# Kernel tuning notes

Hardware: AMD Instinct MI355X
Metric: run time of the kernel (lower is better)

## Reference

```python
import jax, jax.numpy as jnp
import numpy as np

B, S, D, H = 1, 4096, 768, 12
HD = D // H
FF = 4 * D
EPS = 1e-5


def _layer_norm(x, w, b):
    mu = jnp.mean(x, axis=-1, keepdims=True)
    var = jnp.mean((x - mu) ** 2, axis=-1, keepdims=True)
    return (x - mu) * jax.lax.rsqrt(var + EPS) * w + b


def setup_inputs() -> dict:
    key = jax.random.key(0)
    ks = jax.random.split(key, 16)
    s = 0.02
    inp = {
        "hidden_states": jax.random.normal(ks[0], (B, S, D), jnp.float32),
        "attention_mask": jnp.ones((B, S), jnp.int32),
        "ln1_w": jnp.ones((D,), jnp.float32),
        "ln1_b": jnp.zeros((D,), jnp.float32),
        "wq": jax.random.normal(ks[1], (D, D), jnp.float32) * s,
        "bq": jnp.zeros((D,), jnp.float32),
        "wk": jax.random.normal(ks[2], (D, D), jnp.float32) * s,
        "bk": jnp.zeros((D,), jnp.float32),
        "wv": jax.random.normal(ks[3], (D, D), jnp.float32) * s,
        "bv": jnp.zeros((D,), jnp.float32),
        "wo": jax.random.normal(ks[4], (D, D), jnp.float32) * s,
        "bo": jnp.zeros((D,), jnp.float32),
        "ln2_w": jnp.ones((D,), jnp.float32),
        "ln2_b": jnp.zeros((D,), jnp.float32),
        "w_up": jax.random.normal(ks[5], (D, FF), jnp.float32) * s,
        "b_up": jnp.zeros((FF,), jnp.float32),
        "w_down": jax.random.normal(ks[6], (FF, D), jnp.float32) * s,
        "b_down": jnp.zeros((D,), jnp.float32),
    }
    return inp


def reference(hidden_states, attention_mask, ln1_w, ln1_b, wq, bq, wk, bk, wv, bv,
              wo, bo, ln2_w, ln2_b, w_up, b_up, w_down, b_down):
    b, s, _ = hidden_states.shape
    residual = hidden_states
    x = _layer_norm(hidden_states, ln1_w, ln1_b)
    # projections; weights stored [in, out]
    q = (x @ wq + bq).reshape(b, s, H, HD).transpose(0, 2, 1, 3)  # (b,h,s,hd)
    k = (x @ wk + bk).reshape(b, s, H, HD).transpose(0, 2, 1, 3)
    v = (x @ wv + bv).reshape(b, s, H, HD).transpose(0, 2, 1, 3)
    scores = jnp.einsum("bhqd,bhkd->bhqk", q, k) / np.float32(np.sqrt(HD))
    causal = jnp.triu(jnp.ones((s, s), bool), k=1)  # True above diagonal -> mask
    neg_inf = jnp.float32(-jnp.inf)
    scores = jnp.where(causal[None, None, :, :], neg_inf, scores)
    pad = (attention_mask[:, None, None, :] == 0)
    scores = jnp.where(pad, neg_inf, scores)
    weights = jax.nn.softmax(scores, axis=-1)
    attn = jnp.einsum("bhqk,bhkd->bhqd", weights, v)
    attn = attn.transpose(0, 2, 1, 3).reshape(b, s, D)
    hidden = residual + (attn @ wo + bo)
    # FFN
    residual = hidden
    y = _layer_norm(hidden, ln2_w, ln2_b)
    y = jax.nn.gelu(y @ w_up + b_up, approximate=False)
    y = y @ w_down + b_down
    return residual + y
```

## Files before the change

### kernel.cpp

```cpp
#include <hip/hip_runtime.h>
#include <cstdint>
#include <cstddef>


#define S_  4096
#define D_  768
#define H_  12
#define HD_ 64
#define FF_ 3072
#define SD_ (4096 * 768)

typedef short  short8  __attribute__((ext_vector_type(8)));
typedef float  floatx4 __attribute__((ext_vector_type(4)));

__device__ __forceinline__ float bf2f(unsigned short h) {
  union { unsigned int u; float f; } v; v.u = ((unsigned int)h) << 16; return v.f;
}
__device__ __forceinline__ unsigned short f2bf(float f) {
  union { unsigned int u; float f; } v; v.f = f;
  unsigned int u = v.u;
  return (unsigned short)((u + 0x7FFFu + ((u >> 16) & 1u)) >> 16);
}
__device__ __forceinline__ unsigned short f2bf_fast(float f) {
  union { unsigned int u; float f; } v; v.f = f;
  return (unsigned short)((v.u + 0x8000u) >> 16);
}
__device__ __forceinline__ void gload_lds16(const unsigned short* g, unsigned short* l) {
  __builtin_amdgcn_global_load_lds(
      (const __attribute__((address_space(1))) unsigned int*)g,
      (__attribute__((address_space(3))) unsigned int*)l, 16, 0, 0);
}

__global__ void k_cvt_f32(const void* __restrict__ src, float* __restrict__ dst,
                          int n, const int* __restrict__ flagp) {
  const int flag = *flagp;
  for (int i = blockIdx.x * blockDim.x + threadIdx.x; i < n; i += gridDim.x * blockDim.x)
    dst[i] = flag ? ((const float*)src)[i] : bf2f(((const unsigned short*)src)[i]);
}

__global__ __launch_bounds__(256) void k_cvt_t6(
    const void* s0, const void* s1, const void* s2, const void* s3,
    const void* s4, const void* s5,
    unsigned short* d0, unsigned short* d1, unsigned short* d2,
    unsigned short* d3, unsigned short* d4, unsigned short* d5,
    const int* __restrict__ flagp) {
  __shared__ unsigned short T[64 * 65];
  const int flag = *flagp;
  const int b = blockIdx.x;
  const void* src; unsigned short* dst; int K, N, ti;
  if (b < 576) {
    const int seg = b / 144; ti = b - seg * 144; K = 768; N = 768;
    const void* ss[4] = {s0, s1, s2, s3};
    unsigned short* dd[4] = {d0, d1, d2, d3};
    src = ss[seg]; dst = dd[seg];
  } else if (b < 1152) { ti = b - 576;  K = 768;  N = 3072; src = s4; dst = d4; }
  else                 { ti = b - 1152; K = 3072; N = 768;  src = s5; dst = d5; }
  const int nx = N >> 6;
  const int n0 = (ti % nx) * 64, k0 = (ti / nx) * 64;
  const int t = threadIdx.x;
  const int cl = t & 63, rg = t >> 6;
#pragma unroll
  for (int i = 0; i < 16; ++i) {
    const int kl = rg * 16 + i;
    const size_t si = (size_t)(k0 + kl) * N + n0 + cl;
    T[kl * 65 + cl] = flag ? f2bf(((const float*)src)[si]) : ((const unsigned short*)src)[si];
  }
  __syncthreads();
#pragma unroll
  for (int i = 0; i < 16; ++i) {
    const int nl = rg * 16 + i;
    dst[(size_t)(n0 + nl) * K + k0 + cl] = T[cl * 65 + nl];
  }
}

__global__ void k_cvt_params(const void* p0, const void* p1, const void* p2, const void* p3,
                             const void* p4, const void* p5, const void* p6, const void* p7,
                             const void* p8, const void* p9,
                             float* __restrict__ dst, int* __restrict__ flagp) {
  const int flag = (((const unsigned int*)p0)[0] == 0x3F800000u) ? 1 : 0;
  int i = blockIdx.x * 256 + threadIdx.x;
  if (i == 0) *flagp = flag;
  if (i >= 9984) return;
  const void* src; int j;
  if (i < 6912) {
    int seg = i / 768; j = i - seg * 768;
    const void* tbl[9] = {p0, p1, p2, p3, p4, p5, p6, p7, p8};
    src = tbl[seg];
  } else { src = p9; j = i - 6912; }
  dst[i] = flag ? ((const float*)src)[j] : bf2f(((const unsigned short*)src)[j]);
}

__global__ __launch_bounds__(256) void k_ln(const float* __restrict__ x,
                                            const float* __restrict__ w,
                                            const float* __restrict__ b,
                                            unsigned short* __restrict__ out,
                                            const float* __restrict__ bias2,
                                            float* __restrict__ acc) {
  const int row = blockIdx.x, t = threadIdx.x;
  const float* xr = x + (size_t)row * D_;
  float v0 = xr[t], v1 = xr[t + 256], v2 = xr[t + 512];
  float s = v0 + v1 + v2;
  float ss = v0 * v0 + v1 * v1 + v2 * v2;
  for (int off = 32; off > 0; off >>= 1) {
    s  += __shfl_down(s, off);
    ss += __shfl_down(ss, off);
  }
  __shared__ float sb[4], ssb[4];
  const int wid = t >> 6, lane = t & 63;
  if (lane == 0) { sb[wid] = s; ssb[wid] = ss; }
  __syncthreads();
  s  = sb[0] + sb[1] + sb[2] + sb[3];
  ss = ssb[0] + ssb[1] + ssb[2] + ssb[3];
  const float mu   = s * (1.0f / D_);
  const float var  = ss * (1.0f / D_) - mu * mu;
  const float rstd = rsqrtf(var + 1e-5f);
  unsigned short* orow = out + (size_t)row * D_;
  orow[t]       = f2bf((v0 - mu) * rstd * w[t]       + b[t]);
  orow[t + 256] = f2bf((v1 - mu) * rstd * w[t + 256] + b[t + 256]);
  orow[t + 512] = f2bf((v2 - mu) * rstd * w[t + 512] + b[t + 512]);
  if (acc) {
    float* arow = acc + (size_t)row * D_;
    arow[t]       = v0 + bias2[t];
    arow[t + 256] = v1 + bias2[t + 256];
    arow[t + 512] = v2 + bias2[t + 512];
  }
}

template <int TBM, int TBN>
__global__ __launch_bounds__(256) void k_gemm_t(
    const unsigned short* __restrict__ A, const unsigned short* __restrict__ Wt,
    const float* __restrict__ bias, const float* __restrict__ resid,
    void* __restrict__ Cout, int M, int N, int K, int mode, const int* __restrict__ flagp) {
  constexpr int MI = TBM / 32, MJ = TBN / 32;
  __shared__ __align__(16) unsigned short As[2][TBM * 32];
  __shared__ __align__(16) unsigned short Bs[2][TBN * 32];
  const int t = threadIdx.x;
  const int w = t >> 6, lane = t & 63;
  const int quad = lane >> 4, l16 = lane & 15;

  const int gx = gridDim.x, gy = gridDim.y;
  const int nwg = gx * gy * gridDim.z;
  const int id  = blockIdx.x + gx * (blockIdx.y + gy * blockIdx.z);
  const int v   = (id & 7) * (nwg >> 3) + (id >> 3);
  const int vx  = v % gx;
  const int vyz = v / gx;
  const int vy  = vyz % gy;
  const int vz  = vyz / gy;

  const int mb = vy * TBM, nb = vx * TBN;
  const int wm = (w >> 1) * (TBM / 2), wn = (w & 1) * (TBN / 2);
  const int grow = lane >> 2;
  const int gcol = (lane & 3) * 8;

  floatx4 acc[MI][MJ];
#pragma unroll
  for (int i = 0; i < MI; ++i)
#pragma unroll
    for (int j = 0; j < MJ; ++j) acc[i][j] = (floatx4){0.f, 0.f, 0.f, 0.f};

  const int kpb = K / gridDim.z;
  const int kb0 = kpb * vz;
  const int kend = kb0 + kpb;

  auto stage = [&](int buf, int k0) {
#pragma unroll
    for (int r = 0; r < TBM / 64; ++r) {
      const int ch = r * 4 + w;
      gload_lds16(A + (size_t)(mb + ch * 16 + grow) * K + k0 + gcol, &As[buf][ch * 512]);
    }
#pragma unroll
    for (int r = 0; r < TBN / 64; ++r) {
      const int ch = r * 4 + w;
      gload_lds16(Wt + (size_t)(nb + ch * 16 + grow) * K + k0 + gcol, &Bs[buf][ch * 512]);
    }
  };

  stage(0, kb0);
  asm volatile("s_waitcnt vmcnt(0)" ::: "memory");
  __builtin_amdgcn_s_barrier();

  int cur = 0;
  for (int k0 = kb0; k0 < kend; k0 += 32) {
    if (k0 + 32 < kend) stage(cur ^ 1, k0 + 32);

    union { short8 v; uint4 q; } fa[MI], fb[MJ];
#pragma unroll
    for (int i = 0; i < MI; ++i)
      fa[i].q = *(const uint4*)&As[cur][(wm + i * 16 + l16) * 32 + quad * 8];
#pragma unroll
    for (int j = 0; j < MJ; ++j)
      fb[j].q = *(const uint4*)&Bs[cur][(wn + j * 16 + l16) * 32 + quad * 8];
#pragma unroll
    for (int i = 0; i < MI; ++i)
#pragma unroll
      for (int j = 0; j < MJ; ++j)
        acc[i][j] = __builtin_amdgcn_mfma_f32_16x16x32_bf16(fa[i].v, fb[j].v, acc[i][j], 0, 0, 0);

    asm volatile("s_waitcnt vmcnt(0)" ::: "memory");
    __builtin_amdgcn_s_barrier();
    cur ^= 1;
  }

  const int flag = (mode == 3) ? *flagp : 0;
#pragma unroll
  for (int i = 0; i < MI; ++i) {
#pragma unroll
    for (int j = 0; j < MJ; ++j) {
      const int col = nb + wn + j * 16 + l16;
      const float bv = (mode == 6) ? 0.f : bias[col];
#pragma unroll
      for (int r = 0; r < 4; ++r) {
        const int row = mb + wm + i * 16 + quad * 4 + r;
        const size_t idx = (size_t)row * N + col;
        float v = acc[i][j][r] + bv;
        if (mode == 0) {
          ((unsigned short*)Cout)[idx] = f2bf(v);
        } else if (mode == 1) {
          ((float*)Cout)[idx] = v + resid[idx];
        } else if (mode == 2) {
          float g = 0.5f * v * (1.0f + erff(v * 0.70710678118f));
          ((unsigned short*)Cout)[idx] = f2bf(g);
        } else if (mode == 5) {
          unsigned short* q = (unsigned short*)Cout;
          if (col < 768)        q[(size_t)row * 768 + col] = f2bf(v);
          else if (col < 1536) (q + SD_)[(size_t)row * 768 + col - 768] = f2bf(v);
          else                 (q + 2 * (size_t)SD_)[(size_t)(col - 1536) * 4096 + row] = f2bf(v);
        } else if (mode == 6) {
          unsafeAtomicAdd((float*)Cout + idx, v);
        } else {
          v += resid[idx];
          if (flag) ((float*)Cout)[idx] = v;
          else      ((unsigned short*)Cout)[idx] = f2bf(v);
        }
      }
    }
  }
}

__global__ __launch_bounds__(256) void k_out(const float* __restrict__ acc,
                                             const int* __restrict__ flagp,
                                             void* __restrict__ out) {
  const int i = (blockIdx.x * 256 + threadIdx.x) * 4;
  const floatx4 v = *(const floatx4*)(acc + i);
  if (*flagp) {
    *(floatx4*)((float*)out + i) = v;
  } else {
    union { unsigned short e[4]; uint2 u; } p;
#pragma unroll
    for (int e = 0; e < 4; ++e) p.e[e] = f2bf(v[e]);
    *(uint2*)((unsigned short*)out + i) = p.u;
  }
}

#define LK 72
__global__ __launch_bounds__(256) void k_attn_chunk(
    const unsigned short* __restrict__ qb, const unsigned short* __restrict__ kb,
    const unsigned short* __restrict__ vtb, const int* __restrict__ amask,
    unsigned short* __restrict__ Opart, float* __restrict__ Lpart) {
  const int h = blockIdx.y, x = blockIdx.x;
  int g, base;
  if (x < 8)       { g = 0; base = 0; }
  else if (x < 24) { g = 1; base = 8; }
  else if (x < 48) { g = 2; base = 24; }
  else             { g = 3; base = 48; }
  const int rem = x - base;
  const int qt = 8 * g + rem / (g + 1);
  const int c  = rem % (g + 1);
  const int qbase = qt * 128;
  const int kt0 = c * 16;
  const int kt1 = min(kt0 + 16, 2 * qt + 2);

  __shared__ __align__(16) unsigned short Kt[64 * LK];
  __shared__ __align__(16) unsigned short Vt[64 * LK];
  __shared__ __align__(16) unsigned short Ps[128 * LK];
  __shared__ int Mk[64];
  const int t = threadIdx.x;
  const int w = t >> 6, lane = t & 63;
  const int quad = lane >> 4, l16 = lane & 15;
  const int sr = t >> 2, sc = (t & 3) * 16;

  union { short8 v; uint4 q; } qf[2][2];
#pragma unroll
  for (int sub = 0; sub < 2; ++sub) {
    const unsigned short* qp =
        qb + (size_t)(qbase + w * 32 + sub * 16 + l16) * D_ + h * HD_ + quad * 8;
    qf[sub][0].q = *(const uint4*)qp;
    qf[sub][1].q = *(const uint4*)(qp + 32);
  }
  short8 onesB;
#pragma unroll
  for (int e = 0; e < 8; ++e) onesB[e] = (short)0x3F80;
  unsigned short* myP = &Ps[w * 32 * LK];

  floatx4 O[2][4], Lacc[2];
#pragma unroll
  for (int sub = 0; sub < 2; ++sub) {
    Lacc[sub] = (floatx4){0.f, 0.f, 0.f, 0.f};
#pragma unroll
    for (int dc = 0; dc < 4; ++dc) O[sub][dc] = (floatx4){0.f, 0.f, 0.f, 0.f};
  }
  const float sscale = 0.125f * 1.4426950408889634f;
  const int qrow0 = qbase + w * 32 + quad * 4;

  for (int kt = kt0; kt < kt1; ++kt) {
    const int kbase = kt * 64;
    __syncthreads();
    {
      const unsigned short* ks = kb + (size_t)(kbase + sr) * D_ + h * HD_ + sc;
      *(uint4*)&Kt[sr * LK + sc]     = *(const uint4*)ks;
      *(uint4*)&Kt[sr * LK + sc + 8] = *(const uint4*)(ks + 8);
      const unsigned short* vs = vtb + (size_t)(h * HD_ + sr) * S_ + kbase + sc;
      *(uint4*)&Vt[sr * LK + sc]     = *(const uint4*)vs;
      *(uint4*)&Vt[sr * LK + sc + 8] = *(const uint4*)(vs + 8);
      if (t < 64) Mk[t] = amask[kbase + t];
    }
    __syncthreads();

    const bool diag = (kt >= 2 * qt);
#pragma unroll
    for (int kc = 0; kc < 4; ++kc) {
      union { short8 v; uint4 q; } kf[2];
      const unsigned short* p0 = &Kt[(kc * 16 + l16) * LK + quad * 8];
      kf[0].q = *(const uint4*)p0;
      kf[1].q = *(const uint4*)(p0 + 32);
      floatx4 cc[2];
#pragma unroll
      for (int sub = 0; sub < 2; ++sub) {
        cc[sub] = (floatx4){0.f, 0.f, 0.f, 0.f};
        cc[sub] = __builtin_amdgcn_mfma_f32_16x16x32_bf16(qf[sub][0].v, kf[0].v, cc[sub], 0, 0, 0);
        cc[sub] = __builtin_amdgcn_mfma_f32_16x16x32_bf16(qf[sub][1].v, kf[1].v, cc[sub], 0, 0, 0);
      }
      const float mb = (Mk[kc * 16 + l16] == 0) ? -127.f : 0.f;
      const int kg = kbase + kc * 16 + l16;
#pragma unroll
      for (int sub = 0; sub < 2; ++sub)
#pragma unroll
        for (int r = 0; r < 4; ++r) {
          float sv = cc[sub][r] * sscale + mb;
          if (diag && kg > qrow0 + sub * 16 + r) sv = -127.f;
          myP[(sub * 16 + quad * 4 + r) * LK + kc * 16 + l16] = f2bf_fast(exp2f(sv));
        }
    }
    union { short8 v; uint4 q; } pf[2][2];
#pragma unroll
    for (int sub = 0; sub < 2; ++sub) {
      const unsigned short* p0 = &myP[(sub * 16 + l16) * LK + quad * 8];
      pf[sub][0].q = *(const uint4*)p0;
      pf[sub][1].q = *(const uint4*)(p0 + 32);
      Lacc[sub] = __builtin_amdgcn_mfma_f32_16x16x32_bf16(pf[sub][0].v, onesB, Lacc[sub], 0, 0, 0);
      Lacc[sub] = __builtin_amdgcn_mfma_f32_16x16x32_bf16(pf[sub][1].v, onesB, Lacc[sub], 0, 0, 0);
    }
#pragma unroll
    for (int dc = 0; dc < 4; ++dc) {
      union { short8 v; uint4 q; } vf[2];
      const unsigned short* p0 = &Vt[(dc * 16 + l16) * LK + quad * 8];
      vf[0].q = *(const uint4*)p0;
      vf[1].q = *(const uint4*)(p0 + 32);
#pragma unroll
      for (int sub = 0; sub < 2; ++sub) {
        O[sub][dc] = __builtin_amdgcn_mfma_f32_16x16x32_bf16(pf[sub][0].v, vf[0].v, O[sub][dc], 0, 0, 0);
        O[sub][dc] = __builtin_amdgcn_mfma_f32_16x16x32_bf16(pf[sub][1].v, vf[1].v, O[sub][dc], 0, 0, 0);
      }
    }
  }

  const size_t slot = (size_t)h * 80 + x;
#pragma unroll
  for (int sub = 0; sub < 2; ++sub) {
#pragma unroll
    for (int dc = 0; dc < 4; ++dc)
#pragma unroll
      for (int r = 0; r < 4; ++r)
        Opart[slot * 8192 + (w * 32 + sub * 16 + quad * 4 + r) * 64 + dc * 16 + l16] =
            f2bf(O[sub][dc][r]);
    if (l16 == 0) {
#pragma unroll
      for (int r = 0; r < 4; ++r)
        Lpart[slot * 128 + w * 32 + sub * 16 + quad * 4 + r] = Lacc[sub][r];
    }
  }
}

__global__ __launch_bounds__(256) void k_attn_merge(
    const unsigned short* __restrict__ Opart, const float* __restrict__ Lpart,
    unsigned short* __restrict__ ob) {
  const int qt = blockIdx.x, h = blockIdx.y;
  const int t = threadIdx.x;
  const int row = t >> 1, half = (t & 1) * 32;
  const int g = qt >> 3;
  const int nch = g + 1;
  const int cb = h * 80 + 4 * g * (g + 1) + (qt & 7) * (g + 1);
  float L = 0.f;
  float acc[32];
#pragma unroll
  for (int j = 0; j < 32; ++j) acc[j] = 0.f;
  for (int ci = 0; ci < nch; ++ci) {
    L += Lpart[(size_t)(cb + ci) * 128 + row];
    const unsigned short* op = Opart + (size_t)(cb + ci) * 8192 + row * 64 + half;
#pragma unroll
    for (int j4 = 0; j4 < 4; ++j4) {
      union { uint4 v; unsigned short e[8]; } u;
      u.v = *(const uint4*)(op + j4 * 8);
#pragma unroll
      for (int e = 0; e < 8; ++e) acc[j4 * 8 + e] += bf2f(u.e[e]);
    }
  }
  const float inv = 1.f / L;
  unsigned short* orow = ob + (size_t)(qt * 128 + row) * D_ + h * HD_ + half;
#pragma unroll
  for (int j4 = 0; j4 < 4; ++j4) {
    union { uint4 v; unsigned short e[8]; } u;
#pragma unroll
    for (int e = 0; e < 8; ++e) u.e[e] = f2bf(acc[j4 * 8 + e] * inv);
    *(uint4*)(orow + j4 * 8) = u.v;
  }
}

extern "C" void kernel_launch(void* const* d_in, const int* in_sizes, int n_in,
                              void* d_out, int out_size, void* d_ws, size_t ws_size,
                              hipStream_t stream) {
  const void* hidden = d_in[0];
  const int*  amask  = (const int*)d_in[1];
  const void* ln1w = d_in[2];  const void* ln1b = d_in[3];
  const void* wq   = d_in[4];  const void* bq   = d_in[5];
  const void* wk   = d_in[6];  const void* bk   = d_in[7];
  const void* wv   = d_in[8];  const void* bv   = d_in[9];
  const void* wo   = d_in[10]; const void* bo   = d_in[11];
  const void* ln2w = d_in[12]; const void* ln2b = d_in[13];
  const void* wup  = d_in[14]; const void* bup  = d_in[15];
  const void* wdn  = d_in[16]; const void* bdn  = d_in[17];

  char* ws = (char*)d_ws;
  size_t off = 0;
  auto alloc = [&](size_t bytes) {
    char* p = ws + off;
    off += (bytes + 255) & ~(size_t)255;
    return p;
  };
  const size_t SD = (size_t)SD_;
  int*            flagp = (int*)alloc(4);
  float*          h1    = (float*)alloc(SD * 4);
  float*          prm   = (float*)alloc(9984 * 4);
  float*          h2    = (float*)alloc(SD * 4);
  unsigned short* xb    = (unsigned short*)alloc(SD * 2);
  unsigned short* wqkvt = (unsigned short*)alloc((size_t)2304 * 768 * 2);
  unsigned short* wot   = (unsigned short*)alloc((size_t)768 * 768 * 2);
  unsigned short* wupt  = (unsigned short*)alloc((size_t)3072 * 768 * 2);
  unsigned short* wdnt  = (unsigned short*)alloc((size_t)768 * 3072 * 2);
  unsigned short* big   = (unsigned short*)alloc((size_t)S_ * FF_ * 2);
  unsigned short* qb2 = big;
  unsigned short* kb2 = big + SD;
  unsigned short* vtb = big + 2 * SD;
  unsigned short* ab  = big + 3 * SD;
  unsigned short* ffb = big;
  unsigned short* Opart = (unsigned short*)h2;
  float*          Lpart = (float*)((char*)h2 + (size_t)960 * 8192 * 2);

  float* f_ln1w = prm;        float* f_ln1b = prm + 768;
  float* f_ln2w = prm + 1536; float* f_ln2b = prm + 2304;
  float* f_bqkv = prm + 3072; float* f_bo = prm + 5376;
  float* f_bdn = prm + 6144;  float* f_bup = prm + 6912;

  k_cvt_params<<<39, 256, 0, stream>>>(ln1w, ln1b, ln2w, ln2b, bq, bk, bv, bo, bdn, bup,
                                       prm, flagp);
  k_cvt_f32<<<1024, 256, 0, stream>>>(hidden, h1, (int)SD, flagp);
  k_cvt_t6<<<1728, 256, 0, stream>>>(wq, wk, wv, wo, wup, wdn,
                                     wqkvt, wqkvt + 768 * 768, wqkvt + 2 * 768 * 768,
                                     wot, wupt, wdnt, flagp);

  k_ln<<<S_, 256, 0, stream>>>(h1, f_ln1w, f_ln1b, xb, nullptr, nullptr);

  k_gemm_t<128, 128><<<dim3(18, 32), 256, 0, stream>>>(
      xb, wqkvt, f_bqkv, nullptr, qb2, S_, 2304, 768, 5, flagp);

  k_attn_chunk<<<dim3(80, 12), 256, 0, stream>>>(qb2, kb2, vtb, amask, Opart, Lpart);
  k_attn_merge<<<dim3(32, 12), 256, 0, stream>>>(Opart, Lpart, ab);

  k_gemm_t<128, 64><<<dim3(12, 32), 256, 0, stream>>>(
      ab, wot, f_bo, h1, h2, S_, 768, 768, 1, flagp);

  k_ln<<<S_, 256, 0, stream>>>(h2, f_ln2w, f_ln2b, xb, f_bdn, h1);

  k_gemm_t<128, 128><<<dim3(24, 32), 256, 0, stream>>>(
      xb, wupt, f_bup, nullptr, ffb, S_, 3072, 768, 2, flagp);

  k_gemm_t<128, 128><<<dim3(6, 32, 4), 256, 0, stream>>>(
      ffb, wdnt, nullptr, nullptr, h1, S_, 768, 3072, 6, flagp);

  k_out<<<3072, 256, 0, stream>>>(h1, flagp, d_out);
}
```

Before: 392.2 us.

## Prefetch next K/V tile into registers and reorder attention chunk blocks

The attention chunk kernel now loads the next K/V tile and mask into registers while the current tile is computed, then writes them to shared memory at the top of the next iteration. This hides global load latency behind the MFMA work, and one barrier is moved to the end of the loop. The change also reverses the block index so the longest chunks are scheduled first, uses the raw hardware exp2 builtin, and raises wave priority around the MFMA sections. The cost is extra registers for the prefetch buffers, which may reduce occupancy.

Result: no change. 397.0 us (+1.2%).

```diff
diff --git a/kernel.cpp b/kernel.cpp
--- a/kernel.cpp
+++ b/kernel.cpp
@@ -257,7 +257,8 @@
     const unsigned short* __restrict__ qb, const unsigned short* __restrict__ kb,
     const unsigned short* __restrict__ vtb, const int* __restrict__ amask,
     unsigned short* __restrict__ Opart, float* __restrict__ Lpart) {
-  const int h = blockIdx.y, x = blockIdx.x;
+  const int h = blockIdx.y;
+  const int x = 79 - (int)blockIdx.x;
   int g, base;
   if (x < 8)       { g = 0; base = 0; }
   else if (x < 24) { g = 1; base = 8; }
@@ -302,19 +303,29 @@
   const float sscale = 0.125f * 1.4426950408889634f;
   const int qrow0 = qbase + w * 32 + quad * 4;
 
+  uint4 kr0, kr1, vr0, vr1; int mreg = 0;
+  auto prefetch = [&](int kt) {
+    const int kbase = kt * 64;
+    const unsigned short* ks = kb + (size_t)(kbase + sr) * D_ + h * HD_ + sc;
+    kr0 = *(const uint4*)ks;
+    kr1 = *(const uint4*)(ks + 8);
+    const unsigned short* vs = vtb + (size_t)(h * HD_ + sr) * S_ + kbase + sc;
+    vr0 = *(const uint4*)vs;
+    vr1 = *(const uint4*)(vs + 8);
+    if (t < 64) mreg = amask[kbase + t];
+  };
+  prefetch(kt0);
+
   for (int kt = kt0; kt < kt1; ++kt) {
     const int kbase = kt * 64;
+    *(uint4*)&Kt[sr * LK + sc]     = kr0;
+    *(uint4*)&Kt[sr * LK + sc + 8] = kr1;
+    *(uint4*)&Vt[sr * LK + sc]     = vr0;
+    *(uint4*)&Vt[sr * LK + sc + 8] = vr1;
+    if (t < 64) Mk[t] = mreg;
     __syncthreads();
-    {
-      const unsigned short* ks = kb + (size_t)(kbase + sr) * D_ + h * HD_ + sc;
-      *(uint4*)&Kt[sr * LK + sc]     = *(const uint4*)ks;
-      *(uint4*)&Kt[sr * LK + sc + 8] = *(const uint4*)(ks + 8);
-      const unsigned short* vs = vtb + (size_t)(h * HD_ + sr) * S_ + kbase + sc;
-      *(uint4*)&Vt[sr * LK + sc]     = *(const uint4*)vs;
-      *(uint4*)&Vt[sr * LK + sc + 8] = *(const uint4*)(vs + 8);
-      if (t < 64) Mk[t] = amask[kbase + t];
-    }
-    __syncthreads();
+
+    if (kt + 1 < kt1) prefetch(kt + 1);
 
     const bool diag = (kt >= 2 * qt);
 #pragma unroll
@@ -324,12 +335,14 @@
       kf[0].q = *(const uint4*)p0;
       kf[1].q = *(const uint4*)(p0 + 32);
       floatx4 cc[2];
+      __builtin_amdgcn_s_setprio(1);
 #pragma unroll
       for (int sub = 0; sub < 2; ++sub) {
         cc[sub] = (floatx4){0.f, 0.f, 0.f, 0.f};
         cc[sub] = __builtin_amdgcn_mfma_f32_16x16x32_bf16(qf[sub][0].v, kf[0].v, cc[sub], 0, 0, 0);
         cc[sub] = __builtin_amdgcn_mfma_f32_16x16x32_bf16(qf[sub][1].v, kf[1].v, cc[sub], 0, 0, 0);
       }
+      __builtin_amdgcn_s_setprio(0);
       const float mb = (Mk[kc * 16 + l16] == 0) ? -127.f : 0.f;
       const int kg = kbase + kc * 16 + l16;
 #pragma unroll
@@ -338,7 +351,8 @@
         for (int r = 0; r < 4; ++r) {
           float sv = cc[sub][r] * sscale + mb;
           if (diag && kg > qrow0 + sub * 16 + r) sv = -127.f;
-          myP[(sub * 16 + quad * 4 + r) * LK + kc * 16 + l16] = f2bf_fast(exp2f(sv));
+          myP[(sub * 16 + quad * 4 + r) * LK + kc * 16 + l16] =
+              f2bf_fast(__builtin_amdgcn_exp2f(sv));
         }
     }
     union { short8 v; uint4 q; } pf[2][2];
@@ -350,6 +364,7 @@
       Lacc[sub] = __builtin_amdgcn_mfma_f32_16x16x32_bf16(pf[sub][0].v, onesB, Lacc[sub], 0, 0, 0);
       Lacc[sub] = __builtin_amdgcn_mfma_f32_16x16x32_bf16(pf[sub][1].v, onesB, Lacc[sub], 0, 0, 0);
     }
+    __builtin_amdgcn_s_setprio(1);
 #pragma unroll
     for (int dc = 0; dc < 4; ++dc) {
       union { short8 v; uint4 q; } vf[2];
@@ -362,6 +377,8 @@
         O[sub][dc] = __builtin_amdgcn_mfma_f32_16x16x32_bf16(pf[sub][1].v, vf[1].v, O[sub][dc], 0, 0, 0);
       }
     }
+    __builtin_amdgcn_s_setprio(0);
+    __syncthreads();
   }
 
   const size_t slot = (size_t)h * 80 + x;
```

## Load K/V fragments directly from global in attention chunk kernel, drop LDS staging

Applied to the files above, without the earlier changes.

The attention chunk kernel stops staging K, V and the mask in shared memory and removes the two per-tile __syncthreads, so each wave reads its MFMA fragments straight from global memory. The QK^T MFMA operands are swapped so each lane holds one query row, which lets the row sum be accumulated in registers and reduced with shuffles instead of using extra MFMAs against a ones vector. It also adds packed bf16 conversion via inline asm, MFMA priority hints, and reversed block order so the longest chunks launch first. The cost is redundant global/L2 traffic, since all four waves fetch the same K/V tile, and more exposed load latency without staging. The row sum is now taken from the fp32 probabilities before bf16 rounding, so it no longer matches the bf16 values used for the P·V product.

Result: slower. 453.1 us (+15.5%).

```diff
diff --git a/kernel.cpp b/kernel.cpp
--- a/kernel.cpp
+++ b/kernel.cpp
@@ -21,9 +21,10 @@
   unsigned int u = v.u;
   return (unsigned short)((u + 0x7FFFu + ((u >> 16) & 1u)) >> 16);
 }
-__device__ __forceinline__ unsigned short f2bf_fast(float f) {
-  union { unsigned int u; float f; } v; v.f = f;
-  return (unsigned short)((v.u + 0x8000u) >> 16);
+__device__ __forceinline__ unsigned int cvt_pk_bf16(float lo, float hi) {
+  unsigned int r;
+  asm("v_cvt_pk_bf16_f32 %0, %1, %2" : "=v"(r) : "v"(lo), "v"(hi));
+  return r;
 }
 __device__ __forceinline__ void gload_lds16(const unsigned short* g, unsigned short* l) {
   __builtin_amdgcn_global_load_lds(
@@ -257,7 +258,8 @@
     const unsigned short* __restrict__ qb, const unsigned short* __restrict__ kb,
     const unsigned short* __restrict__ vtb, const int* __restrict__ amask,
     unsigned short* __restrict__ Opart, float* __restrict__ Lpart) {
-  const int h = blockIdx.y, x = blockIdx.x;
+  const int h = blockIdx.y;
+  const int x = 79 - (int)blockIdx.x;
   int g, base;
   if (x < 8)       { g = 0; base = 0; }
   else if (x < 24) { g = 1; base = 8; }
@@ -270,14 +272,10 @@
   const int kt0 = c * 16;
   const int kt1 = min(kt0 + 16, 2 * qt + 2);
 
-  __shared__ __align__(16) unsigned short Kt[64 * LK];
-  __shared__ __align__(16) unsigned short Vt[64 * LK];
   __shared__ __align__(16) unsigned short Ps[128 * LK];
-  __shared__ int Mk[64];
   const int t = threadIdx.x;
   const int w = t >> 6, lane = t & 63;
   const int quad = lane >> 4, l16 = lane & 15;
-  const int sr = t >> 2, sc = (t & 3) * 16;
 
   union { short8 v; uint4 q; } qf[2][2];
 #pragma unroll
@@ -287,81 +285,85 @@
     qf[sub][0].q = *(const uint4*)qp;
     qf[sub][1].q = *(const uint4*)(qp + 32);
   }
-  short8 onesB;
-#pragma unroll
-  for (int e = 0; e < 8; ++e) onesB[e] = (short)0x3F80;
   unsigned short* myP = &Ps[w * 32 * LK];
 
-  floatx4 O[2][4], Lacc[2];
-#pragma unroll
-  for (int sub = 0; sub < 2; ++sub) {
-    Lacc[sub] = (floatx4){0.f, 0.f, 0.f, 0.f};
+  floatx4 O[2][4];
+  float lsum[2] = {0.f, 0.f};
+#pragma unroll
+  for (int sub = 0; sub < 2; ++sub)
 #pragma unroll
     for (int dc = 0; dc < 4; ++dc) O[sub][dc] = (floatx4){0.f, 0.f, 0.f, 0.f};
-  }
   const float sscale = 0.125f * 1.4426950408889634f;
-  const int qrow0 = qbase + w * 32 + quad * 4;
+  const int qrow0 = qbase + w * 32 + l16;
 
   for (int kt = kt0; kt < kt1; ++kt) {
     const int kbase = kt * 64;
-    __syncthreads();
-    {
-      const unsigned short* ks = kb + (size_t)(kbase + sr) * D_ + h * HD_ + sc;
-      *(uint4*)&Kt[sr * LK + sc]     = *(const uint4*)ks;
-      *(uint4*)&Kt[sr * LK + sc + 8] = *(const uint4*)(ks + 8);
-      const unsigned short* vs = vtb + (size_t)(h * HD_ + sr) * S_ + kbase + sc;
-      *(uint4*)&Vt[sr * LK + sc]     = *(const uint4*)vs;
-      *(uint4*)&Vt[sr * LK + sc + 8] = *(const uint4*)(vs + 8);
-      if (t < 64) Mk[t] = amask[kbase + t];
-    }
-    __syncthreads();
-
     const bool diag = (kt >= 2 * qt);
+
 #pragma unroll
     for (int kc = 0; kc < 4; ++kc) {
       union { short8 v; uint4 q; } kf[2];
-      const unsigned short* p0 = &Kt[(kc * 16 + l16) * LK + quad * 8];
-      kf[0].q = *(const uint4*)p0;
-      kf[1].q = *(const uint4*)(p0 + 32);
+      const unsigned short* kp =
+          kb + (size_t)(kbase + kc * 16 + l16) * D_ + h * HD_ + quad * 8;
+      kf[0].q = *(const uint4*)kp;
+      kf[1].q = *(const uint4*)(kp + 32);
       floatx4 cc[2];
+      __builtin_amdgcn_s_setprio(1);
 #pragma unroll
       for (int sub = 0; sub < 2; ++sub) {
         cc[sub] = (floatx4){0.f, 0.f, 0.f, 0.f};
-        cc[sub] = __builtin_amdgcn_mfma_f32_16x16x32_bf16(qf[sub][0].v, kf[0].v, cc[sub], 0, 0, 0);
-        cc[sub] = __builtin_amdgcn_mfma_f32_16x16x32_bf16(qf[sub][1].v, kf[1].v, cc[sub], 0, 0, 0);
+        cc[sub] = __builtin_amdgcn_mfma_f32_16x16x32_bf16(kf[0].v, qf[sub][0].v, cc[sub], 0, 0, 0);
+        cc[sub] = __builtin_amdgcn_mfma_f32_16x16x32_bf16(kf[1].v, qf[sub][1].v, cc[sub], 0, 0, 0);
       }
-      const float mb = (Mk[kc * 16 + l16] == 0) ? -127.f : 0.f;
-      const int kg = kbase + kc * 16 + l16;
-#pragma unroll
-      for (int sub = 0; sub < 2; ++sub)
+      __builtin_amdgcn_s_setprio(0);
+      const int kg0 = kbase + kc * 16 + quad * 4;
+      const int4 m4 = *(const int4*)(amask + kg0);
+#pragma unroll
+      for (int sub = 0; sub < 2; ++sub) {
+        const int qr = qrow0 + sub * 16;
+        float p[4];
 #pragma unroll
         for (int r = 0; r < 4; ++r) {
-          float sv = cc[sub][r] * sscale + mb;
-          if (diag && kg > qrow0 + sub * 16 + r) sv = -127.f;
-          myP[(sub * 16 + quad * 4 + r) * LK + kc * 16 + l16] = f2bf_fast(exp2f(sv));
+          const float e = __builtin_amdgcn_exp2f(cc[sub][r] * sscale);
+          const int mv = (r == 0) ? m4.x : (r == 1) ? m4.y : (r == 2) ? m4.z : m4.w;
+          const bool keep = (mv != 0) && (!diag || (kg0 + r <= qr));
+          p[r] = keep ? e : 0.f;
+          lsum[sub] += p[r];
         }
-    }
+        const unsigned int d0 = cvt_pk_bf16(p[0], p[1]);
+        const unsigned int d1 = cvt_pk_bf16(p[2], p[3]);
+        *(uint2*)&myP[(sub * 16 + l16) * LK + kc * 16 + quad * 4] = (uint2){d0, d1};
+      }
+    }
+
     union { short8 v; uint4 q; } pf[2][2];
 #pragma unroll
     for (int sub = 0; sub < 2; ++sub) {
       const unsigned short* p0 = &myP[(sub * 16 + l16) * LK + quad * 8];
       pf[sub][0].q = *(const uint4*)p0;
       pf[sub][1].q = *(const uint4*)(p0 + 32);
-      Lacc[sub] = __builtin_amdgcn_mfma_f32_16x16x32_bf16(pf[sub][0].v, onesB, Lacc[sub], 0, 0, 0);
-      Lacc[sub] = __builtin_amdgcn_mfma_f32_16x16x32_bf16(pf[sub][1].v, onesB, Lacc[sub], 0, 0, 0);
     }
 #pragma unroll
     for (int dc = 0; dc < 4; ++dc) {
       union { short8 v; uint4 q; } vf[2];
-      const unsigned short* p0 = &Vt[(dc * 16 + l16) * LK + quad * 8];
-      vf[0].q = *(const uint4*)p0;
-      vf[1].q = *(const uint4*)(p0 + 32);
+      const unsigned short* vp =
+          vtb + (size_t)(h * HD_ + dc * 16 + l16) * S_ + kbase + quad * 8;
+      vf[0].q = *(const uint4*)vp;
+      vf[1].q = *(const uint4*)(vp + 32);
+      __builtin_amdgcn_s_setprio(1);
 #pragma unroll
       for (int sub = 0; sub < 2; ++sub) {
         O[sub][dc] = __builtin_amdgcn_mfma_f32_16x16x32_bf16(pf[sub][0].v, vf[0].v, O[sub][dc], 0, 0, 0);
         O[sub][dc] = __builtin_amdgcn_mfma_f32_16x16x32_bf16(pf[sub][1].v, vf[1].v, O[sub][dc], 0, 0, 0);
       }
-    }
+      __builtin_amdgcn_s_setprio(0);
+    }
+  }
+
+#pragma unroll
+  for (int sub = 0; sub < 2; ++sub) {
+    lsum[sub] += __shfl_xor(lsum[sub], 16);
+    lsum[sub] += __shfl_xor(lsum[sub], 32);
   }
 
   const size_t slot = (size_t)h * 80 + x;
@@ -373,11 +375,8 @@
       for (int r = 0; r < 4; ++r)
         Opart[slot * 8192 + (w * 32 + sub * 16 + quad * 4 + r) * 64 + dc * 16 + l16] =
             f2bf(O[sub][dc][r]);
-    if (l16 == 0) {
-#pragma unroll
-      for (int r = 0; r < 4; ++r)
-        Lpart[slot * 128 + w * 32 + sub * 16 + quad * 4 + r] = Lacc[sub][r];
-    }
+    if (lane < 16)
+      Lpart[slot * 128 + w * 32 + sub * 16 + lane] = lsum[sub];
   }
 }
 
```
